# Performance work log

Measured on AMD Instinct MI355X. Metric: run time of the kernel, lower is better.

The kernel has to match this reference:

```python
import jax, jax.numpy as jnp
from jax import lax
import numpy as np

PI = np.float32(np.pi)
DN = ('NCHW', 'OIHW', 'NCHW')
PAD = [(1, 1), (1, 1)]


def setup_inputs() -> dict:
    key = jax.random.key(0)
    k1, k2 = jax.random.split(key, 2)
    B, C, H, W_ = 8, 64, 256, 256
    OUT, K = 64, 8
    x = jax.random.normal(k1, (B, C, H, W_), dtype=jnp.float32)
    # kaiming-normal-like scale for 3x3 conv weights
    W = jax.random.normal(k2, (K, OUT, C, 3, 3), dtype=jnp.float32) * np.float32(np.sqrt(2.0 / (C * 9)))
    b = jnp.zeros((K, OUT), dtype=jnp.float32)  # nn.init.zeros_(conv.bias)
    return {"x": x, "W": W, "b": b}


def reference(x, W, b):
    B, C, H, Wd = x.shape
    K = W.shape[0]
    sx = jnp.array([[1, 0, -1], [2, 0, -2], [1, 0, -1]], dtype=jnp.float32)
    sy = jnp.array([[1, 2, 1], [0, 0, 0], [-1, -2, -1]], dtype=jnp.float32)
    kx = jnp.tile(sx[None, None], (C, 1, 1, 1))  # (C,1,3,3) depthwise
    ky = jnp.tile(sy[None, None], (C, 1, 1, 1))
    grad_x = lax.conv_general_dilated(x, kx, (1, 1), PAD, dimension_numbers=DN, feature_group_count=C)
    grad_y = lax.conv_general_dilated(x, ky, (1, 1), PAD, dimension_numbers=DN, feature_group_count=C)
    theta = jnp.arctan2(grad_y, grad_x)
    # ((theta+pi)/(2pi)*K).long() % K ; values >= 0 so trunc == floor
    q = ((theta + PI) / (2 * PI) * K).astype(jnp.int32) % K  # (B,C,H,W)
    out = jnp.zeros((B, W.shape[1], H, Wd), dtype=x.dtype)
    for k in range(K):
        mask = (q == k).astype(x.dtype)
        fk = lax.conv_general_dilated(x * mask, W[k], (1, 1), PAD, dimension_numbers=DN)
        out = out + fk + b[k][None, :, None, None]
    return out / K
```

## Files before the change

### kernel.cpp

```cpp
#include <hip/hip_runtime.h>
#include <math.h>


#define TH 16
#define TW 32

typedef __attribute__((ext_vector_type(8)))  short    short8;
typedef __attribute__((ext_vector_type(16))) float    f32x16;
typedef __attribute__((ext_vector_type(4)))  unsigned u32x4;

__device__ __forceinline__ float atanf_fdlibm(float x) {
#pragma clang fp contract(off)
    const float atanhi0 = 4.6364760399e-01f, atanhi1 = 7.8539812565e-01f,
                atanhi2 = 9.8279368877e-01f, atanhi3 = 1.5707962513e+00f;
    const float atanlo0 = 5.0121582440e-09f, atanlo1 = 3.7748947079e-08f,
                atanlo2 = 3.4473217170e-08f, atanlo3 = 7.5497894159e-08f;
    const float aT0 = 3.3333334327e-01f, aT1 = -2.0000000298e-01f, aT2 = 1.4285714924e-01f,
                aT3 = -1.1111110449e-01f, aT4 = 9.0908870101e-02f, aT5 = -7.6918758452e-02f,
                aT6 = 6.6610731184e-02f, aT7 = -5.8335702866e-02f, aT8 = 4.9768779427e-02f,
                aT9 = -3.6531571299e-02f, aT10 = 1.6285819933e-02f;

    int hx = __float_as_int(x);
    int ix = hx & 0x7fffffff;
    int id;
    if (ix >= 0x4c800000) {
        if (ix > 0x7f800000) return x + x;
        return (hx > 0) ? (atanhi3 + atanlo3) : (-atanhi3 - atanlo3);
    }
    if (ix < 0x3ee00000) {
        if (ix < 0x31000000) return x;
        id = -1;
    } else {
        x = fabsf(x);
        if (ix < 0x3f980000) {
            if (ix < 0x3f300000) { id = 0; x = (2.0f * x - 1.0f) / (2.0f + x); }
            else                 { id = 1; x = (x - 1.0f) / (x + 1.0f); }
        } else {
            if (ix < 0x401c0000) { id = 2; x = (x - 1.5f) / (1.0f + 1.5f * x); }
            else                 { id = 3; x = -1.0f / x; }
        }
    }
    float z = x * x;
    float w = z * z;
    float s1 = z * (aT0 + w * (aT2 + w * (aT4 + w * (aT6 + w * (aT8 + w * aT10)))));
    float s2 = w * (aT1 + w * (aT3 + w * (aT5 + w * (aT7 + w * aT9))));
    if (id < 0) return x - x * (s1 + s2);
    float r;
    if      (id == 0) r = atanhi0 - ((x * (s1 + s2) - atanlo0) - x);
    else if (id == 1) r = atanhi1 - ((x * (s1 + s2) - atanlo1) - x);
    else if (id == 2) r = atanhi2 - ((x * (s1 + s2) - atanlo2) - x);
    else              r = atanhi3 - ((x * (s1 + s2) - atanlo3) - x);
    return (hx < 0) ? -r : r;
}

__device__ __forceinline__ float atan2f_fdlibm(float y, float x) {
#pragma clang fp contract(off)
    const float tiny = 1.0e-30f;
    const float pi_o_4 = 7.8539818525e-01f;
    const float pi_o_2 = 1.5707963705e+00f;
    const float pi     = 3.1415927410e+00f;
    const float pi_lo  = -8.7422776573e-08f;

    int hx = __float_as_int(x), hy = __float_as_int(y);
    int ix = hx & 0x7fffffff, iy = hy & 0x7fffffff;
    if (ix > 0x7f800000 || iy > 0x7f800000) return x + y;
    if (hx == 0x3f800000) return atanf_fdlibm(y);
    int m = ((hy >> 31) & 1) | ((hx >> 30) & 2);

    if (iy == 0) {
        switch (m) {
            case 0:
            case 1:  return y;
            case 2:  return  pi + tiny;
            default: return -pi - tiny;
        }
    }
    if (ix == 0) return (hy < 0) ? (-pi_o_2 - tiny) : (pi_o_2 + tiny);
    if (ix == 0x7f800000) {
        if (iy == 0x7f800000) {
            switch (m) {
                case 0:  return  pi_o_4 + tiny;
                case 1:  return -pi_o_4 - tiny;
                case 2:  return  3.0f * pi_o_4 + tiny;
                default: return -3.0f * pi_o_4 - tiny;
            }
        } else {
            switch (m) {
                case 0:  return  0.0f;
                case 1:  return -0.0f;
                case 2:  return  pi + tiny;
                default: return -pi - tiny;
            }
        }
    }
    if (iy == 0x7f800000) return (hy < 0) ? (-pi_o_2 - tiny) : (pi_o_2 + tiny);

    int k = (iy - ix) >> 23;
    float z;
    int mm = m;
    if (k > 26)                    { z = pi_o_2 + 0.5f * pi_lo; mm &= 1; }
    else if (hx < 0 && k < -26)    { z = 0.0f; }
    else                           { z = atanf_fdlibm(fabsf(y / x)); }

    switch (mm) {
        case 0:  return z;
        case 1:  return -z;
        case 2:  return pi - (z - pi_lo);
        default: return (z - pi_lo) - pi;
    }
}

__device__ __forceinline__ int bin8(float gy, float gx) {
#pragma clang fp contract(off)
    float th = atan2f_fdlibm(gy, gx);
    float t  = th + 3.14159274101257324f;
    float u  = t / 6.28318548202514648f;
    u = u * 8.0f;
    return ((int)u) & 7;
}

__device__ __forceinline__ int bin8_bf(float gy, float gx) {
#pragma clang fp contract(off)
    const float aT0 = 3.3333334327e-01f, aT1 = -2.0000000298e-01f, aT2 = 1.4285714924e-01f,
                aT3 = -1.1111110449e-01f, aT4 = 9.0908870101e-02f, aT5 = -7.6918758452e-02f,
                aT6 = 6.6610731184e-02f, aT7 = -5.8335702866e-02f, aT8 = 4.9768779427e-02f,
                aT9 = -3.6531571299e-02f, aT10 = 1.6285819933e-02f;
    const float pi    = 3.1415927410e+00f;
    const float pi_lo = -8.7422776573e-08f;
    const float pio2  = 1.5707963705e+00f;

    int hx = __float_as_int(gx), hy = __float_as_int(gy);
    int ix = hx & 0x7fffffff,   iy = hy & 0x7fffffff;
    int m  = ((hy >> 31) & 1) | ((hx >> 30) & 2);

    float q  = fabsf(gy / gx);
    int   iq = __float_as_int(q);

    bool lt04375 = iq < 0x3ee00000;
    bool lt06875 = iq < 0x3f300000;
    bool lt11875 = iq < 0x3f980000;
    bool lt24375 = iq < 0x401c0000;

    float n0 = 2.0f * q - 1.0f, d0 = 2.0f + q;
    float n1 = q - 1.0f,        d1 = q + 1.0f;
    float n2 = q - 1.5f,        d2 = 1.0f + 1.5f * q;
    float num = lt04375 ? q    : lt06875 ? n0 : lt11875 ? n1 : lt24375 ? n2 : -1.0f;
    float den = lt04375 ? 1.0f : lt06875 ? d0 : lt11875 ? d1 : lt24375 ? d2 : q;
    float hi  = lt06875 ? 4.6364760399e-01f : lt11875 ? 7.8539812565e-01f
              : lt24375 ? 9.8279368877e-01f : 1.5707962513e+00f;
    float lo  = lt06875 ? 5.0121582440e-09f : lt11875 ? 3.7748947079e-08f
              : lt24375 ? 3.4473217170e-08f : 7.5497894159e-08f;

    float a  = num / den;
    float z2 = a * a;
    float w2 = z2 * z2;
    float s1 = z2 * (aT0 + w2 * (aT2 + w2 * (aT4 + w2 * (aT6 + w2 * (aT8 + w2 * aT10)))));
    float s2 = w2 * (aT1 + w2 * (aT3 + w2 * (aT5 + w2 * (aT7 + w2 * aT9))));
    float S  = s1 + s2;
    float resm1 = a - a * S;
    float resid = hi - ((a * S - lo) - a);
    float zr = lt04375 ? resm1 : resid;
    zr = (iq >= 0x4c800000) ? (1.5707962513e+00f + 7.5497894159e-08f) : zr;

    int  k    = (iy - ix) >> 23;
    bool kbig = k > 26;
    float z   = kbig ? (pio2 + 0.5f * pi_lo) : zr;
    z = (hx < 0 && k < -26) ? 0.0f : z;
    int mm = kbig ? (m & 1) : m;

    float w  = z - pi_lo;
    float r2 = pi - w;
    float r3 = w - pi;
    float res = (mm == 0) ? z : (mm == 1) ? -z : (mm == 2) ? r2 : r3;
    res = (ix == 0) ? ((hy < 0) ? -pio2 : pio2) : res;
    float piy = (m == 2) ? pi : (m == 3) ? -pi : gy;
    res = (iy == 0) ? piy : res;

    float t = res + 3.14159274101257324f;
    float u = t / 6.28318548202514648f;
    u = u * 8.0f;
    return ((int)u) & 7;
}

__device__ __forceinline__ unsigned rne_bf16_bits(float f) {
    unsigned u = __float_as_uint(f);
    return (u + 0x7fffu + ((u >> 16) & 1u)) >> 16;
}

__global__ __launch_bounds__(256)
void bin_kernel(const float* __restrict__ x, unsigned* __restrict__ pwg) {
    __shared__ float rs[3][260];
    const int w    = threadIdx.x;
    const int hrow = blockIdx.x;
    const int img  = blockIdx.y;
    const float* xim = x + ((size_t)img << 16);
    #pragma unroll
    for (int r = 0; r < 3; ++r) {
        int gh = hrow - 1 + r;
        float v = 0.f;
        if ((unsigned)gh < 256u) v = xim[(gh << 8) + w];
        rs[r][w + 1] = v;
        if (w == 0) { rs[r][0] = 0.f; rs[r][257] = 0.f; }
    }
    __syncthreads();
    int q; unsigned hv;
    {
#pragma clang fp contract(off)
        float a0 = rs[0][w], a1 = rs[0][w + 1], a2 = rs[0][w + 2];
        float m0 = rs[1][w],                    m2 = rs[1][w + 2];
        float z0 = rs[2][w], z1 = rs[2][w + 1], z2 = rs[2][w + 2];
        float gx = ((((a0 - a2) + 2.0f * m0) - 2.0f * m2) + z0) - z2;
        float gy = ((((a0 + 2.0f * a1) + a2) - z0) - 2.0f * z1) - z2;
        q  = bin8_bf(gy, gx);
        hv = rne_bf16_bits(rs[1][w + 1]);
    }
    pwg[((size_t)img << 16) + (hrow << 8) + w] = (hv << 16) | (unsigned)q;
}

__global__ void prep_w2(const float* __restrict__ Wg, short* __restrict__ wsw) {
    int tid = blockIdx.x * 256 + threadIdx.x;
    if (tid >= 4096) return;
    int c = tid >> 6, o = tid & 63;
    for (int t = 0; t < 9; ++t)
        #pragma unroll
        for (int k = 0; k < 8; ++k)
            wsw[((((c * 10 + t) << 6) + o) << 3) + k] =
                (short)rne_bf16_bits(Wg[(((k << 6) + o) * 64 + c) * 9 + t]);
    #pragma unroll
    for (int k = 0; k < 8; ++k)
        wsw[((((c * 10 + 9) << 6) + o) << 3) + k] = 0;
}

__device__ __forceinline__ void build_oh(unsigned pv, u32x4* dst) {
    unsigned q  = pv & 7u;
    unsigned hv = (q & 1u) ? (pv & 0xffff0000u) : (pv >> 16);
    unsigned s2 = q >> 1;
    u32x4 oh;
    oh.x = (s2 == 0u) ? hv : 0u;
    oh.y = (s2 == 1u) ? hv : 0u;
    oh.z = (s2 == 2u) ? hv : 0u;
    oh.w = (s2 == 3u) ? hv : 0u;
    *dst = oh;
}

__global__ __launch_bounds__(256, 2)
void dirconv_mfma2(const unsigned* __restrict__ pwg,
                   const short*    __restrict__ wsw,
                   const float*    __restrict__ bg,
                   float*          __restrict__ out) {
    __shared__ u32x4 pwx[2][648];
    __shared__ u32x4 wl2[2][640];
    __shared__ float bsum[64];

    const int tid  = threadIdx.x;
    const int wave = tid >> 6;
    const int lane = tid & 63;
    const int h    = lane >> 5;
    const int l31  = lane & 31;
    const int bb   = blockIdx.z;
    const int h0   = blockIdx.y * TH;
    const int w0c  = blockIdx.x * TW;

    if (tid < 64) {
        float s = 0.f;
        #pragma unroll
        for (int k = 0; k < 8; ++k) s += bg[k * 64 + tid];
        bsum[tid] = s;
    }

    f32x16 acc[2][4];
    #pragma unroll
    for (int i = 0; i < 2; ++i)
        #pragma unroll
        for (int j = 0; j < 4; ++j)
            acc[i][j] = (f32x16)0.f;

    int rro[5], c2o[5];
    #pragma unroll
    for (int s = 0; s < 5; ++s) {
        int t = 2 * s + h;
        int t3 = t / 3;
        rro[s] = (t <= 8) ? t3 : 0;
        c2o[s] = (t <= 8) ? (t - t3 * 3) : 0;
    }

    {
        const u32x4* wsrc = (const u32x4*)wsw;
        wl2[0][tid]       = wsrc[tid];
        wl2[0][tid + 256] = wsrc[tid + 256];
        if (tid < 128) wl2[0][tid + 512] = wsrc[tid + 512];
        const unsigned* pimg = pwg + ((size_t)(bb * 64) << 16);
        #pragma unroll
        for (int rd = 0; rd < 3; ++rd) {
            int idx = tid + rd * 256;
            if (idx < 612) {
                int r = idx / 34, cc2 = idx - r * 34;
                int gh = h0 + r - 1, gw = w0c + cc2 - 1;
                unsigned pv = 0;
                if ((unsigned)gh < 256u && (unsigned)gw < 256u)
                    pv = pimg[(gh << 8) + gw];
                build_oh(pv, &pwx[0][r * 36 + cc2]);
            }
        }
    }
    __syncthreads();

    for (int c = 0; c < 64; ++c) {
        const int cb = c & 1, nb = cb ^ 1;
        u32x4 wv0 = (u32x4)0u, wv1 = (u32x4)0u, wv2 = (u32x4)0u;
        unsigned pv0 = 0, pv1 = 0, pv2 = 0;
        const bool more = (c < 63);

        if (more) {
            const u32x4* wsrc = (const u32x4*)(wsw + (size_t)(c + 1) * 5120);
            wv0 = wsrc[tid];
            wv1 = wsrc[tid + 256];
            if (tid < 128) wv2 = wsrc[tid + 512];
            const unsigned* pimg = pwg + ((size_t)(bb * 64 + c + 1) << 16);
            {   int idx = tid;       int r = idx / 34, cc2 = idx - r * 34;
                int gh = h0 + r - 1, gw = w0c + cc2 - 1;
                if ((unsigned)gh < 256u && (unsigned)gw < 256u) pv0 = pimg[(gh << 8) + gw]; }
            {   int idx = tid + 256; int r = idx / 34, cc2 = idx - r * 34;
                int gh = h0 + r - 1, gw = w0c + cc2 - 1;
                if ((unsigned)gh < 256u && (unsigned)gw < 256u) pv1 = pimg[(gh << 8) + gw]; }
            if (tid < 100) {
                int idx = tid + 512; int r = idx / 34, cc2 = idx - r * 34;
                int gh = h0 + r - 1, gw = w0c + cc2 - 1;
                if ((unsigned)gh < 256u && (unsigned)gw < 256u) pv2 = pimg[(gh << 8) + gw]; }
        }

        const u32x4* pb = &pwx[cb][0];
        const u32x4* wb = &wl2[cb][0];
        auto mfma_step = [&](int s) {
            const int t = 2 * s + h;
            short8 a0 = __builtin_bit_cast(short8, wb[t * 64 + l31]);
            short8 a1 = __builtin_bit_cast(short8, wb[t * 64 + 32 + l31]);
            #pragma unroll
            for (int nf = 0; nf < 4; ++nf) {
                int py = wave * 4 + nf;
                short8 bf = __builtin_bit_cast(short8,
                                pb[(py + rro[s]) * 36 + l31 + c2o[s]]);
                acc[0][nf] = __builtin_amdgcn_mfma_f32_32x32x16_bf16(a0, bf, acc[0][nf], 0, 0, 0);
                acc[1][nf] = __builtin_amdgcn_mfma_f32_32x32x16_bf16(a1, bf, acc[1][nf], 0, 0, 0);
            }
        };

        __builtin_amdgcn_s_setprio(1);
        mfma_step(0);
        mfma_step(1);
        __builtin_amdgcn_s_setprio(0);
        if (more) {
            wl2[nb][tid]       = wv0;
            wl2[nb][tid + 256] = wv1;
            if (tid < 128) wl2[nb][tid + 512] = wv2;
        }
        __builtin_amdgcn_s_setprio(1);
        mfma_step(2);
        __builtin_amdgcn_s_setprio(0);
        if (more) {
            {   int idx = tid;       int r = idx / 34, cc2 = idx - r * 34;
                build_oh(pv0, &pwx[nb][r * 36 + cc2]); }
            {   int idx = tid + 256; int r = idx / 34, cc2 = idx - r * 34;
                build_oh(pv1, &pwx[nb][r * 36 + cc2]); }
        }
        __builtin_amdgcn_s_setprio(1);
        mfma_step(3);
        __builtin_amdgcn_s_setprio(0);
        if (more && tid < 100) {
            int idx = tid + 512; int r = idx / 34, cc2 = idx - r * 34;
            build_oh(pv2, &pwx[nb][r * 36 + cc2]);
        }
        __builtin_amdgcn_s_setprio(1);
        mfma_step(4);
        __builtin_amdgcn_s_setprio(0);
        __syncthreads();
    }

    float* ob = out + ((size_t)bb << 22);
    #pragma unroll
    for (int mf = 0; mf < 2; ++mf)
        #pragma unroll
        for (int nf = 0; nf < 4; ++nf) {
            int py = wave * 4 + nf;
            #pragma unroll
            for (int reg = 0; reg < 16; ++reg) {
                int o = mf * 32 + (reg & 3) + 8 * (reg >> 2) + 4 * h;
                ob[((size_t)o << 16) + ((h0 + py) << 8) + (w0c + l31)] =
                    (acc[mf][nf][reg] + bsum[o]) * 0.125f;
            }
        }
}

__global__ __launch_bounds__(256, 2)
void dirconv_fb(const float* __restrict__ x,
                const float* __restrict__ Wg,
                const float* __restrict__ bg,
                float* __restrict__ out) {
    __shared__ float    xs[20 * 37];
    __shared__ unsigned pw[18 * 36];
    __shared__ short    wl[64][128];
    __shared__ float    bsum[64];

    const int tid  = threadIdx.x;
    const int wave = tid >> 6;
    const int lane = tid & 63;
    const int h    = lane >> 5;
    const int l31  = lane & 31;
    const int bb   = blockIdx.z;
    const int h0   = blockIdx.y * TH;
    const int w0   = blockIdx.x * TW;

    if (tid < 64) {
        float s = 0.f;
        #pragma unroll
        for (int k = 0; k < 8; ++k) s += bg[k * 64 + tid];
        bsum[tid] = s;
    }

    f32x16 acc[2][4];
    #pragma unroll
    for (int i = 0; i < 2; ++i)
        #pragma unroll
        for (int j = 0; j < 4; ++j)
            acc[i][j] = (f32x16)0.f;

    const int swz0 = l31 & 7;

    for (int c = 0; c < 64; ++c) {
        __syncthreads();
        const float* xc = x + ((size_t)(bb * 64 + c) << 16);
        for (int idx = tid; idx < 720; idx += 256) {
            int r = idx / 36, cc = idx - r * 36;
            int gh = h0 + r - 2, gw = w0 + cc - 2;
            float v = 0.f;
            if ((unsigned)gh < 256u && (unsigned)gw < 256u)
                v = xc[(gh << 8) + gw];
            xs[r * 37 + cc] = v;
        }
        for (int pair = tid; pair < 512; pair += 256) {
            int k = pair >> 6, o = pair & 63;
            const float* g = Wg + ((size_t)((k << 6) + o) * 64 + c) * 9;
            #pragma unroll
            for (int t = 0; t < 9; ++t)
                wl[o][((t ^ (o & 7)) << 3) + k] = (short)rne_bf16_bits(g[t]);
        }
        if (tid < 64) {
            int o = tid;
            #pragma unroll
            for (int e = 0; e < 8; ++e) wl[o][((9 ^ (o & 7)) << 3) + e] = 0;
        }
        __syncthreads();

        for (int idx = tid; idx < 612; idx += 256) {
            int r = idx / 34, cc = idx - r * 34;
            const float* p0 = &xs[r * 37 + cc];
            int q; unsigned hv;
            {
#pragma clang fp contract(off)
                float a0 = p0[0],  a1 = p0[1],  a2 = p0[2];
                float m0 = p0[37],              m2 = p0[39];
                float z0 = p0[74], z1 = p0[75], z2 = p0[76];
                float gx = ((((a0 - a2) + 2.0f * m0) - 2.0f * m2) + z0) - z2;
                float gy = ((((a0 + 2.0f * a1) + a2) - z0) - 2.0f * z1) - z2;
                q  = bin8(gy, gx);
                hv = rne_bf16_bits(p0[38]);
            }
            pw[r * 36 + cc] = (hv << 16) | (unsigned)q;
        }
        __syncthreads();

        #pragma unroll
        for (int s = 0; s < 5; ++s) {
            const int t = 2 * s + h;
            short8 a0 = *(const short8*)&wl[l31     ][(t ^ swz0) << 3];
            short8 a1 = *(const short8*)&wl[32 + l31][(t ^ swz0) << 3];
            const int t3 = t / 3;
            const int dy = t3 - 1, dx = t - t3 * 3 - 1;
            const bool val = (t <= 8);
            #pragma unroll
            for (int nf = 0; nf < 4; ++nf) {
                int py = wave * 4 + nf;
                int rr = val ? (py + 1 + dy) : 0;
                int c2 = val ? (l31 + 1 + dx) : 0;
                unsigned pv = pw[rr * 36 + c2];
                pv = val ? pv : 0u;
                unsigned q   = pv & 7u;
                unsigned hhi = pv & 0xffff0000u;
                unsigned hlo = pv >> 16;
                u32x4 bw;
                bw.x = (q == 0u ? hlo : 0u) | (q == 1u ? hhi : 0u);
                bw.y = (q == 2u ? hlo : 0u) | (q == 3u ? hhi : 0u);
                bw.z = (q == 4u ? hlo : 0u) | (q == 5u ? hhi : 0u);
                bw.w = (q == 6u ? hlo : 0u) | (q == 7u ? hhi : 0u);
                short8 bf = __builtin_bit_cast(short8, bw);
                acc[0][nf] = __builtin_amdgcn_mfma_f32_32x32x16_bf16(a0, bf, acc[0][nf], 0, 0, 0);
                acc[1][nf] = __builtin_amdgcn_mfma_f32_32x32x16_bf16(a1, bf, acc[1][nf], 0, 0, 0);
            }
        }
    }

    float* ob = out + ((size_t)bb << 22);
    #pragma unroll
    for (int mf = 0; mf < 2; ++mf)
        #pragma unroll
        for (int nf = 0; nf < 4; ++nf) {
            int py = wave * 4 + nf;
            #pragma unroll
            for (int reg = 0; reg < 16; ++reg) {
                int o = mf * 32 + (reg & 3) + 8 * (reg >> 2) + 4 * h;
                ob[((size_t)o << 16) + ((h0 + py) << 8) + (w0 + l31)] =
                    (acc[mf][nf][reg] + bsum[o]) * 0.125f;
            }
        }
}

extern "C" void kernel_launch(void* const* d_in, const int* in_sizes, int n_in,
                              void* d_out, int out_size, void* d_ws, size_t ws_size,
                              hipStream_t stream) {
    const float* x  = (const float*)d_in[0];
    const float* Wg = (const float*)d_in[1];
    const float* bg = (const float*)d_in[2];
    float* out = (float*)d_out;

    dim3 grid(256 / TW, 256 / TH, 8);
    dim3 block(256);

    const size_t pw_bytes   = (size_t)8 * 64 * 256 * 256 * 4;
    const size_t wsw2_bytes = (size_t)64 * 10 * 64 * 8 * 2;

    if (ws_size >= pw_bytes + wsw2_bytes) {
        unsigned* pwg = (unsigned*)d_ws;
        short*    wsw = (short*)((char*)d_ws + pw_bytes);
        bin_kernel<<<dim3(256, 512, 1), 256, 0, stream>>>(x, pwg);
        prep_w2<<<16, 256, 0, stream>>>(Wg, wsw);
        dirconv_mfma2<<<grid, block, 0, stream>>>(pwg, wsw, bg, out);
    } else {
        dirconv_fb<<<grid, block, 0, stream>>>(x, Wg, bg, out);
    }
}
```

Before: 416.0 us.

## Halve conv tile height, load weights directly into registers, batch bin kernel rows

The main conv kernel now works on 8-row tiles with half the accumulators per wave, targeting 3 blocks per CU. It drops the LDS weight double-buffer and instead loads each MFMA step's A fragments straight from global memory into ping-pong registers, one step ahead. The bin kernel now processes 16 rows per block from an 18-row LDS tile, which cuts redundant halo loads. In exchange, each tile reloads a larger share of halo rows and every step depends on global weight-load latency being hidden behind the MFMAs.

```diff
diff --git a/kernel.cpp b/kernel.cpp
--- a/kernel.cpp
+++ b/kernel.cpp
@@ -2,7 +2,7 @@
 #include <math.h>
 
 
-#define TH 16
+#define TH 8
 #define TW 32
 
 typedef __attribute__((ext_vector_type(8)))  short    short8;
@@ -188,33 +188,34 @@
 }
 
 __global__ __launch_bounds__(256)
-void bin_kernel(const float* __restrict__ x, unsigned* __restrict__ pwg) {
-    __shared__ float rs[3][260];
-    const int w    = threadIdx.x;
-    const int hrow = blockIdx.x;
-    const int img  = blockIdx.y;
+void bin_kernel2(const float* __restrict__ x, unsigned* __restrict__ pwg) {
+    __shared__ float rs[18][260];
+    const int w   = threadIdx.x;
+    const int r0  = blockIdx.x << 4;
+    const int img = blockIdx.y;
     const float* xim = x + ((size_t)img << 16);
     #pragma unroll
-    for (int r = 0; r < 3; ++r) {
-        int gh = hrow - 1 + r;
-        float v = 0.f;
-        if ((unsigned)gh < 256u) v = xim[(gh << 8) + w];
-        rs[r][w + 1] = v;
-        if (w == 0) { rs[r][0] = 0.f; rs[r][257] = 0.f; }
-    }
+    for (int r = 0; r < 18; ++r) {
+        int gh = r0 + r - 1;
+        rs[r][w + 1] = ((unsigned)gh < 256u) ? xim[(gh << 8) + w] : 0.f;
+    }
+    if (w < 18) { rs[w][0] = 0.f; rs[w][257] = 0.f; }
     __syncthreads();
-    int q; unsigned hv;
-    {
+    unsigned* orow = pwg + ((size_t)img << 16) + (r0 << 8) + w;
+    for (int rr = 0; rr < 16; ++rr) {
+        int q; unsigned hv;
+        {
 #pragma clang fp contract(off)
-        float a0 = rs[0][w], a1 = rs[0][w + 1], a2 = rs[0][w + 2];
-        float m0 = rs[1][w],                    m2 = rs[1][w + 2];
-        float z0 = rs[2][w], z1 = rs[2][w + 1], z2 = rs[2][w + 2];
-        float gx = ((((a0 - a2) + 2.0f * m0) - 2.0f * m2) + z0) - z2;
-        float gy = ((((a0 + 2.0f * a1) + a2) - z0) - 2.0f * z1) - z2;
-        q  = bin8_bf(gy, gx);
-        hv = rne_bf16_bits(rs[1][w + 1]);
-    }
-    pwg[((size_t)img << 16) + (hrow << 8) + w] = (hv << 16) | (unsigned)q;
+            float a0 = rs[rr][w],     a1 = rs[rr][w + 1],     a2 = rs[rr][w + 2];
+            float m0 = rs[rr + 1][w],                         m2 = rs[rr + 1][w + 2];
+            float z0 = rs[rr + 2][w], z1 = rs[rr + 2][w + 1], z2 = rs[rr + 2][w + 2];
+            float gx = ((((a0 - a2) + 2.0f * m0) - 2.0f * m2) + z0) - z2;
+            float gy = ((((a0 + 2.0f * a1) + a2) - z0) - 2.0f * z1) - z2;
+            q  = bin8_bf(gy, gx);
+            hv = rne_bf16_bits(rs[rr + 1][w + 1]);
+        }
+        orow[rr << 8] = (hv << 16) | (unsigned)q;
+    }
 }
 
 __global__ void prep_w2(const float* __restrict__ Wg, short* __restrict__ wsw) {
@@ -243,13 +244,65 @@
     *dst = oh;
 }
 
-__global__ __launch_bounds__(256, 2)
-void dirconv_mfma2(const unsigned* __restrict__ pwg,
+#define WLOAD(DST, CC, SS) do {                                                      \
+    int t_ = 2 * (SS) + h;                                                           \
+    const u32x4* wp_ = (const u32x4*)(wsw + (size_t)((((CC) * 10 + t_) << 6)) * 8);  \
+    DST[0] = wp_[l31];                                                               \
+    DST[1] = wp_[32 + l31];                                                          \
+} while (0)
+
+#define MSTEP(P, SS) do {                                                            \
+    __builtin_amdgcn_s_setprio(1);                                                   \
+    short8 a0_ = __builtin_bit_cast(short8, P[0]);                                   \
+    short8 a1_ = __builtin_bit_cast(short8, P[1]);                                   \
+    _Pragma("unroll")                                                                \
+    for (int nf = 0; nf < 2; ++nf) {                                                 \
+        int py_ = (wave << 1) + nf;                                                  \
+        short8 bf_ = __builtin_bit_cast(short8,                                      \
+                         pb[(py_ + rro[SS]) * 36 + l31 + c2o[SS]]);                  \
+        acc[0][nf] = __builtin_amdgcn_mfma_f32_32x32x16_bf16(a0_, bf_, acc[0][nf], 0, 0, 0); \
+        acc[1][nf] = __builtin_amdgcn_mfma_f32_32x32x16_bf16(a1_, bf_, acc[1][nf], 0, 0, 0); \
+    }                                                                                \
+    __builtin_amdgcn_s_setprio(0);                                                   \
+} while (0)
+
+#define CBODY(C, P, Q) do {                                                          \
+    const int  cb_ = (C) & 1, nb_ = cb_ ^ 1;                                         \
+    const int  cn_ = ((C) < 63) ? (C) + 1 : 63;                                      \
+    const bool more_ = (C) < 63;                                                     \
+    unsigned pv0_ = 0, pv1_ = 0;                                                     \
+    if (more_) {                                                                     \
+        const unsigned* pimg_ = pwg + ((size_t)(bb * 64 + (C) + 1) << 16);           \
+        { int r_ = tid / 34, cc_ = tid - r_ * 34;                                    \
+          int gh_ = h0 + r_ - 1, gw_ = w0c + cc_ - 1;                                \
+          if ((unsigned)gh_ < 256u && (unsigned)gw_ < 256u)                          \
+              pv0_ = pimg_[(gh_ << 8) + gw_]; }                                      \
+        if (tid < 84) { int i_ = tid + 256; int r_ = i_ / 34, cc_ = i_ - r_ * 34;    \
+          int gh_ = h0 + r_ - 1, gw_ = w0c + cc_ - 1;                                \
+          if ((unsigned)gh_ < 256u && (unsigned)gw_ < 256u)                          \
+              pv1_ = pimg_[(gh_ << 8) + gw_]; }                                      \
+    }                                                                                \
+    const u32x4* pb = &pwx[cb_][0];                                                  \
+    MSTEP(P, 0);  WLOAD(P, (C), 2);                                                  \
+    MSTEP(Q, 1);  WLOAD(Q, (C), 3);                                                  \
+    MSTEP(P, 2);  WLOAD(P, (C), 4);                                                  \
+    if (more_) {                                                                     \
+        { int r_ = tid / 34, cc_ = tid - r_ * 34;                                    \
+          build_oh(pv0_, &pwx[nb_][r_ * 36 + cc_]); }                                \
+        if (tid < 84) { int i_ = tid + 256; int r_ = i_ / 34, cc_ = i_ - r_ * 34;    \
+          build_oh(pv1_, &pwx[nb_][r_ * 36 + cc_]); }                                \
+    }                                                                                \
+    MSTEP(Q, 3);  WLOAD(Q, cn_, 0);                                                  \
+    MSTEP(P, 4);  WLOAD(P, cn_, 1);                                                  \
+    __syncthreads();                                                                 \
+} while (0)
+
+__global__ __launch_bounds__(256, 3)
+void dirconv_mfma3(const unsigned* __restrict__ pwg,
                    const short*    __restrict__ wsw,
                    const float*    __restrict__ bg,
                    float*          __restrict__ out) {
-    __shared__ u32x4 pwx[2][648];
-    __shared__ u32x4 wl2[2][640];
+    __shared__ u32x4 pwx[2][360];
     __shared__ float bsum[64];
 
     const int tid  = threadIdx.x;
@@ -268,11 +321,11 @@
         bsum[tid] = s;
     }
 
-    f32x16 acc[2][4];
+    f32x16 acc[2][2];
     #pragma unroll
     for (int i = 0; i < 2; ++i)
         #pragma unroll
-        for (int j = 0; j < 4; ++j)
+        for (int j = 0; j < 2; ++j)
             acc[i][j] = (f32x16)0.f;
 
     int rro[5], c2o[5];
@@ -284,104 +337,36 @@
         c2o[s] = (t <= 8) ? (t - t3 * 3) : 0;
     }
 
+    u32x4 A0[2], A1[2];
+
     {
-        const u32x4* wsrc = (const u32x4*)wsw;
-        wl2[0][tid]       = wsrc[tid];
-        wl2[0][tid + 256] = wsrc[tid + 256];
-        if (tid < 128) wl2[0][tid + 512] = wsrc[tid + 512];
         const unsigned* pimg = pwg + ((size_t)(bb * 64) << 16);
-        #pragma unroll
-        for (int rd = 0; rd < 3; ++rd) {
-            int idx = tid + rd * 256;
-            if (idx < 612) {
-                int r = idx / 34, cc2 = idx - r * 34;
-                int gh = h0 + r - 1, gw = w0c + cc2 - 1;
-                unsigned pv = 0;
-                if ((unsigned)gh < 256u && (unsigned)gw < 256u)
-                    pv = pimg[(gh << 8) + gw];
-                build_oh(pv, &pwx[0][r * 36 + cc2]);
-            }
-        }
+        { int r = tid / 34, cc2 = tid - r * 34;
+          int gh = h0 + r - 1, gw = w0c + cc2 - 1;
+          unsigned pv = 0;
+          if ((unsigned)gh < 256u && (unsigned)gw < 256u) pv = pimg[(gh << 8) + gw];
+          build_oh(pv, &pwx[0][r * 36 + cc2]); }
+        if (tid < 84) { int i = tid + 256; int r = i / 34, cc2 = i - r * 34;
+          int gh = h0 + r - 1, gw = w0c + cc2 - 1;
+          unsigned pv = 0;
+          if ((unsigned)gh < 256u && (unsigned)gw < 256u) pv = pimg[(gh << 8) + gw];
+          build_oh(pv, &pwx[0][r * 36 + cc2]); }
+        WLOAD(A0, 0, 0);
+        WLOAD(A1, 0, 1);
     }
     __syncthreads();
 
-    for (int c = 0; c < 64; ++c) {
-        const int cb = c & 1, nb = cb ^ 1;
-        u32x4 wv0 = (u32x4)0u, wv1 = (u32x4)0u, wv2 = (u32x4)0u;
-        unsigned pv0 = 0, pv1 = 0, pv2 = 0;
-        const bool more = (c < 63);
-
-        if (more) {
-            const u32x4* wsrc = (const u32x4*)(wsw + (size_t)(c + 1) * 5120);
-            wv0 = wsrc[tid];
-            wv1 = wsrc[tid + 256];
-            if (tid < 128) wv2 = wsrc[tid + 512];
-            const unsigned* pimg = pwg + ((size_t)(bb * 64 + c + 1) << 16);
-            {   int idx = tid;       int r = idx / 34, cc2 = idx - r * 34;
-                int gh = h0 + r - 1, gw = w0c + cc2 - 1;
-                if ((unsigned)gh < 256u && (unsigned)gw < 256u) pv0 = pimg[(gh << 8) + gw]; }
-            {   int idx = tid + 256; int r = idx / 34, cc2 = idx - r * 34;
-                int gh = h0 + r - 1, gw = w0c + cc2 - 1;
-                if ((unsigned)gh < 256u && (unsigned)gw < 256u) pv1 = pimg[(gh << 8) + gw]; }
-            if (tid < 100) {
-                int idx = tid + 512; int r = idx / 34, cc2 = idx - r * 34;
-                int gh = h0 + r - 1, gw = w0c + cc2 - 1;
-                if ((unsigned)gh < 256u && (unsigned)gw < 256u) pv2 = pimg[(gh << 8) + gw]; }
-        }
-
-        const u32x4* pb = &pwx[cb][0];
-        const u32x4* wb = &wl2[cb][0];
-        auto mfma_step = [&](int s) {
-            const int t = 2 * s + h;
-            short8 a0 = __builtin_bit_cast(short8, wb[t * 64 + l31]);
-            short8 a1 = __builtin_bit_cast(short8, wb[t * 64 + 32 + l31]);
-            #pragma unroll
-            for (int nf = 0; nf < 4; ++nf) {
-                int py = wave * 4 + nf;
-                short8 bf = __builtin_bit_cast(short8,
-                                pb[(py + rro[s]) * 36 + l31 + c2o[s]]);
-                acc[0][nf] = __builtin_amdgcn_mfma_f32_32x32x16_bf16(a0, bf, acc[0][nf], 0, 0, 0);
-                acc[1][nf] = __builtin_amdgcn_mfma_f32_32x32x16_bf16(a1, bf, acc[1][nf], 0, 0, 0);
-            }
-        };
-
-        __builtin_amdgcn_s_setprio(1);
-        mfma_step(0);
-        mfma_step(1);
-        __builtin_amdgcn_s_setprio(0);
-        if (more) {
-            wl2[nb][tid]       = wv0;
-            wl2[nb][tid + 256] = wv1;
-            if (tid < 128) wl2[nb][tid + 512] = wv2;
-        }
-        __builtin_amdgcn_s_setprio(1);
-        mfma_step(2);
-        __builtin_amdgcn_s_setprio(0);
-        if (more) {
-            {   int idx = tid;       int r = idx / 34, cc2 = idx - r * 34;
-                build_oh(pv0, &pwx[nb][r * 36 + cc2]); }
-            {   int idx = tid + 256; int r = idx / 34, cc2 = idx - r * 34;
-                build_oh(pv1, &pwx[nb][r * 36 + cc2]); }
-        }
-        __builtin_amdgcn_s_setprio(1);
-        mfma_step(3);
-        __builtin_amdgcn_s_setprio(0);
-        if (more && tid < 100) {
-            int idx = tid + 512; int r = idx / 34, cc2 = idx - r * 34;
-            build_oh(pv2, &pwx[nb][r * 36 + cc2]);
-        }
-        __builtin_amdgcn_s_setprio(1);
-        mfma_step(4);
-        __builtin_amdgcn_s_setprio(0);
-        __syncthreads();
+    for (int c2 = 0; c2 < 64; c2 += 2) {
+        CBODY(c2,     A0, A1);
+        CBODY(c2 + 1, A1, A0);
     }
 
     float* ob = out + ((size_t)bb << 22);
     #pragma unroll
     for (int mf = 0; mf < 2; ++mf)
         #pragma unroll
-        for (int nf = 0; nf < 4; ++nf) {
-            int py = wave * 4 + nf;
+        for (int nf = 0; nf < 2; ++nf) {
+            int py = (wave << 1) + nf;
             #pragma unroll
             for (int reg = 0; reg < 16; ++reg) {
                 int o = mf * 32 + (reg & 3) + 8 * (reg >> 2) + 4 * h;
@@ -407,8 +392,8 @@
     const int h    = lane >> 5;
     const int l31  = lane & 31;
     const int bb   = blockIdx.z;
-    const int h0   = blockIdx.y * TH;
-    const int w0   = blockIdx.x * TW;
+    const int h0   = blockIdx.y * 16;
+    const int w0   = blockIdx.x * 32;
 
     if (tid < 64) {
         float s = 0.f;
@@ -522,19 +507,16 @@
     const float* bg = (const float*)d_in[2];
     float* out = (float*)d_out;
 
-    dim3 grid(256 / TW, 256 / TH, 8);
-    dim3 block(256);
-
     const size_t pw_bytes   = (size_t)8 * 64 * 256 * 256 * 4;
     const size_t wsw2_bytes = (size_t)64 * 10 * 64 * 8 * 2;
 
     if (ws_size >= pw_bytes + wsw2_bytes) {
         unsigned* pwg = (unsigned*)d_ws;
         short*    wsw = (short*)((char*)d_ws + pw_bytes);
-        bin_kernel<<<dim3(256, 512, 1), 256, 0, stream>>>(x, pwg);
+        bin_kernel2<<<dim3(16, 512, 1), 256, 0, stream>>>(x, pwg);
         prep_w2<<<16, 256, 0, stream>>>(Wg, wsw);
-        dirconv_mfma2<<<grid, block, 0, stream>>>(pwg, wsw, bg, out);
+        dirconv_mfma3<<<dim3(256 / TW, 256 / TH, 8), 256, 0, stream>>>(pwg, wsw, bg, out);
     } else {
-        dirconv_fb<<<grid, block, 0, stream>>>(x, Wg, bg, out);
-    }
-}
+        dirconv_fb<<<dim3(8, 16, 8), 256, 0, stream>>>(x, Wg, bg, out);
+    }
+}
```

After: 417.7 us. About the same (+0.4%).

## Halve conv tile height for four blocks per CU and batch bin rows

Applied to the files above, without the earlier changes.

The MFMA conv kernel now uses 8-row tiles with half the accumulators per wave and launch bounds of 4 blocks per CU, so more blocks fit per CU and latency hiding improves. The interleaved staging of next-channel data between MFMA steps is replaced by a plain loop followed by a single LDS store phase. The bin kernel now processes 16 rows per block from a shared 18-row strip, cutting redundant halo loads and block count. The trade-off is more halo overhead per output in the conv tiles and less overlap of LDS writes with MFMA work.

```diff
diff --git a/kernel.cpp b/kernel.cpp
--- a/kernel.cpp
+++ b/kernel.cpp
@@ -2,7 +2,7 @@
 #include <math.h>
 
 
-#define TH 16
+#define TH 8
 #define TW 32
 
 typedef __attribute__((ext_vector_type(8)))  short    short8;
@@ -188,33 +188,34 @@
 }
 
 __global__ __launch_bounds__(256)
-void bin_kernel(const float* __restrict__ x, unsigned* __restrict__ pwg) {
-    __shared__ float rs[3][260];
-    const int w    = threadIdx.x;
-    const int hrow = blockIdx.x;
-    const int img  = blockIdx.y;
+void bin_kernel2(const float* __restrict__ x, unsigned* __restrict__ pwg) {
+    __shared__ float rs[18][260];
+    const int w   = threadIdx.x;
+    const int r0  = blockIdx.x << 4;
+    const int img = blockIdx.y;
     const float* xim = x + ((size_t)img << 16);
     #pragma unroll
-    for (int r = 0; r < 3; ++r) {
-        int gh = hrow - 1 + r;
-        float v = 0.f;
-        if ((unsigned)gh < 256u) v = xim[(gh << 8) + w];
-        rs[r][w + 1] = v;
-        if (w == 0) { rs[r][0] = 0.f; rs[r][257] = 0.f; }
-    }
+    for (int r = 0; r < 18; ++r) {
+        int gh = r0 + r - 1;
+        rs[r][w + 1] = ((unsigned)gh < 256u) ? xim[(gh << 8) + w] : 0.f;
+    }
+    if (w < 18) { rs[w][0] = 0.f; rs[w][257] = 0.f; }
     __syncthreads();
-    int q; unsigned hv;
-    {
+    unsigned* orow = pwg + ((size_t)img << 16) + (r0 << 8) + w;
+    for (int rr = 0; rr < 16; ++rr) {
+        int q; unsigned hv;
+        {
 #pragma clang fp contract(off)
-        float a0 = rs[0][w], a1 = rs[0][w + 1], a2 = rs[0][w + 2];
-        float m0 = rs[1][w],                    m2 = rs[1][w + 2];
-        float z0 = rs[2][w], z1 = rs[2][w + 1], z2 = rs[2][w + 2];
-        float gx = ((((a0 - a2) + 2.0f * m0) - 2.0f * m2) + z0) - z2;
-        float gy = ((((a0 + 2.0f * a1) + a2) - z0) - 2.0f * z1) - z2;
-        q  = bin8_bf(gy, gx);
-        hv = rne_bf16_bits(rs[1][w + 1]);
-    }
-    pwg[((size_t)img << 16) + (hrow << 8) + w] = (hv << 16) | (unsigned)q;
+            float a0 = rs[rr][w],     a1 = rs[rr][w + 1],     a2 = rs[rr][w + 2];
+            float m0 = rs[rr + 1][w],                         m2 = rs[rr + 1][w + 2];
+            float z0 = rs[rr + 2][w], z1 = rs[rr + 2][w + 1], z2 = rs[rr + 2][w + 2];
+            float gx = ((((a0 - a2) + 2.0f * m0) - 2.0f * m2) + z0) - z2;
+            float gy = ((((a0 + 2.0f * a1) + a2) - z0) - 2.0f * z1) - z2;
+            q  = bin8_bf(gy, gx);
+            hv = rne_bf16_bits(rs[rr + 1][w + 1]);
+        }
+        orow[rr << 8] = (hv << 16) | (unsigned)q;
+    }
 }
 
 __global__ void prep_w2(const float* __restrict__ Wg, short* __restrict__ wsw) {
@@ -243,12 +244,12 @@
     *dst = oh;
 }
 
-__global__ __launch_bounds__(256, 2)
-void dirconv_mfma2(const unsigned* __restrict__ pwg,
+__global__ __launch_bounds__(256, 4)
+void dirconv_mfma4(const unsigned* __restrict__ pwg,
                    const short*    __restrict__ wsw,
                    const float*    __restrict__ bg,
                    float*          __restrict__ out) {
-    __shared__ u32x4 pwx[2][648];
+    __shared__ u32x4 pwx[2][360];
     __shared__ u32x4 wl2[2][640];
     __shared__ float bsum[64];
 
@@ -268,11 +269,11 @@
         bsum[tid] = s;
     }
 
-    f32x16 acc[2][4];
+    f32x16 acc[2][2];
     #pragma unroll
     for (int i = 0; i < 2; ++i)
         #pragma unroll
-        for (int j = 0; j < 4; ++j)
+        for (int j = 0; j < 2; ++j)
             acc[i][j] = (f32x16)0.f;
 
     int rro[5], c2o[5];
@@ -283,6 +284,10 @@
         rro[s] = (t <= 8) ? t3 : 0;
         c2o[s] = (t <= 8) ? (t - t3 * 3) : 0;
     }
+
+    const int r0_ = tid / 34, c0_ = tid - r0_ * 34;
+    const int i1_ = tid + 256;
+    const int r1_ = i1_ / 34, c1_ = i1_ - r1_ * 34;
 
     {
         const u32x4* wsrc = (const u32x4*)wsw;
@@ -290,26 +295,26 @@
         wl2[0][tid + 256] = wsrc[tid + 256];
         if (tid < 128) wl2[0][tid + 512] = wsrc[tid + 512];
         const unsigned* pimg = pwg + ((size_t)(bb * 64) << 16);
-        #pragma unroll
-        for (int rd = 0; rd < 3; ++rd) {
-            int idx = tid + rd * 256;
-            if (idx < 612) {
-                int r = idx / 34, cc2 = idx - r * 34;
-                int gh = h0 + r - 1, gw = w0c + cc2 - 1;
-                unsigned pv = 0;
-                if ((unsigned)gh < 256u && (unsigned)gw < 256u)
-                    pv = pimg[(gh << 8) + gw];
-                build_oh(pv, &pwx[0][r * 36 + cc2]);
-            }
+        {
+            int gh = h0 + r0_ - 1, gw = w0c + c0_ - 1;
+            unsigned pv = 0;
+            if ((unsigned)gh < 256u && (unsigned)gw < 256u) pv = pimg[(gh << 8) + gw];
+            build_oh(pv, &pwx[0][r0_ * 36 + c0_]);
+        }
+        if (tid < 84) {
+            int gh = h0 + r1_ - 1, gw = w0c + c1_ - 1;
+            unsigned pv = 0;
+            if ((unsigned)gh < 256u && (unsigned)gw < 256u) pv = pimg[(gh << 8) + gw];
+            build_oh(pv, &pwx[0][r1_ * 36 + c1_]);
         }
     }
     __syncthreads();
 
     for (int c = 0; c < 64; ++c) {
         const int cb = c & 1, nb = cb ^ 1;
+        const bool more = (c < 63);
         u32x4 wv0 = (u32x4)0u, wv1 = (u32x4)0u, wv2 = (u32x4)0u;
-        unsigned pv0 = 0, pv1 = 0, pv2 = 0;
-        const bool more = (c < 63);
+        unsigned pv0 = 0, pv1 = 0;
 
         if (more) {
             const u32x4* wsrc = (const u32x4*)(wsw + (size_t)(c + 1) * 5120);
@@ -317,62 +322,42 @@
             wv1 = wsrc[tid + 256];
             if (tid < 128) wv2 = wsrc[tid + 512];
             const unsigned* pimg = pwg + ((size_t)(bb * 64 + c + 1) << 16);
-            {   int idx = tid;       int r = idx / 34, cc2 = idx - r * 34;
-                int gh = h0 + r - 1, gw = w0c + cc2 - 1;
-                if ((unsigned)gh < 256u && (unsigned)gw < 256u) pv0 = pimg[(gh << 8) + gw]; }
-            {   int idx = tid + 256; int r = idx / 34, cc2 = idx - r * 34;
-                int gh = h0 + r - 1, gw = w0c + cc2 - 1;
-                if ((unsigned)gh < 256u && (unsigned)gw < 256u) pv1 = pimg[(gh << 8) + gw]; }
-            if (tid < 100) {
-                int idx = tid + 512; int r = idx / 34, cc2 = idx - r * 34;
-                int gh = h0 + r - 1, gw = w0c + cc2 - 1;
-                if ((unsigned)gh < 256u && (unsigned)gw < 256u) pv2 = pimg[(gh << 8) + gw]; }
+            {
+                int gh = h0 + r0_ - 1, gw = w0c + c0_ - 1;
+                if ((unsigned)gh < 256u && (unsigned)gw < 256u) pv0 = pimg[(gh << 8) + gw];
+            }
+            if (tid < 84) {
+                int gh = h0 + r1_ - 1, gw = w0c + c1_ - 1;
+                if ((unsigned)gh < 256u && (unsigned)gw < 256u) pv1 = pimg[(gh << 8) + gw];
+            }
         }
 
         const u32x4* pb = &pwx[cb][0];
         const u32x4* wb = &wl2[cb][0];
-        auto mfma_step = [&](int s) {
+        #pragma unroll
+        for (int s = 0; s < 5; ++s) {
             const int t = 2 * s + h;
             short8 a0 = __builtin_bit_cast(short8, wb[t * 64 + l31]);
             short8 a1 = __builtin_bit_cast(short8, wb[t * 64 + 32 + l31]);
+            __builtin_amdgcn_s_setprio(1);
             #pragma unroll
-            for (int nf = 0; nf < 4; ++nf) {
-                int py = wave * 4 + nf;
+            for (int nf = 0; nf < 2; ++nf) {
+                int py = (wave << 1) + nf;
                 short8 bf = __builtin_bit_cast(short8,
                                 pb[(py + rro[s]) * 36 + l31 + c2o[s]]);
                 acc[0][nf] = __builtin_amdgcn_mfma_f32_32x32x16_bf16(a0, bf, acc[0][nf], 0, 0, 0);
                 acc[1][nf] = __builtin_amdgcn_mfma_f32_32x32x16_bf16(a1, bf, acc[1][nf], 0, 0, 0);
             }
-        };
-
-        __builtin_amdgcn_s_setprio(1);
-        mfma_step(0);
-        mfma_step(1);
-        __builtin_amdgcn_s_setprio(0);
+            __builtin_amdgcn_s_setprio(0);
+        }
+
         if (more) {
             wl2[nb][tid]       = wv0;
             wl2[nb][tid + 256] = wv1;
             if (tid < 128) wl2[nb][tid + 512] = wv2;
-        }
-        __builtin_amdgcn_s_setprio(1);
-        mfma_step(2);
-        __builtin_amdgcn_s_setprio(0);
-        if (more) {
-            {   int idx = tid;       int r = idx / 34, cc2 = idx - r * 34;
-                build_oh(pv0, &pwx[nb][r * 36 + cc2]); }
-            {   int idx = tid + 256; int r = idx / 34, cc2 = idx - r * 34;
-                build_oh(pv1, &pwx[nb][r * 36 + cc2]); }
-        }
-        __builtin_amdgcn_s_setprio(1);
-        mfma_step(3);
-        __builtin_amdgcn_s_setprio(0);
-        if (more && tid < 100) {
-            int idx = tid + 512; int r = idx / 34, cc2 = idx - r * 34;
-            build_oh(pv2, &pwx[nb][r * 36 + cc2]);
-        }
-        __builtin_amdgcn_s_setprio(1);
-        mfma_step(4);
-        __builtin_amdgcn_s_setprio(0);
+            build_oh(pv0, &pwx[nb][r0_ * 36 + c0_]);
+            if (tid < 84) build_oh(pv1, &pwx[nb][r1_ * 36 + c1_]);
+        }
         __syncthreads();
     }
 
@@ -380,8 +365,8 @@
     #pragma unroll
     for (int mf = 0; mf < 2; ++mf)
         #pragma unroll
-        for (int nf = 0; nf < 4; ++nf) {
-            int py = wave * 4 + nf;
+        for (int nf = 0; nf < 2; ++nf) {
+            int py = (wave << 1) + nf;
             #pragma unroll
             for (int reg = 0; reg < 16; ++reg) {
                 int o = mf * 32 + (reg & 3) + 8 * (reg >> 2) + 4 * h;
@@ -407,8 +392,8 @@
     const int h    = lane >> 5;
     const int l31  = lane & 31;
     const int bb   = blockIdx.z;
-    const int h0   = blockIdx.y * TH;
-    const int w0   = blockIdx.x * TW;
+    const int h0   = blockIdx.y * 16;
+    const int w0   = blockIdx.x * 32;
 
     if (tid < 64) {
         float s = 0.f;
@@ -522,19 +507,16 @@
     const float* bg = (const float*)d_in[2];
     float* out = (float*)d_out;
 
-    dim3 grid(256 / TW, 256 / TH, 8);
-    dim3 block(256);
-
     const size_t pw_bytes   = (size_t)8 * 64 * 256 * 256 * 4;
     const size_t wsw2_bytes = (size_t)64 * 10 * 64 * 8 * 2;
 
     if (ws_size >= pw_bytes + wsw2_bytes) {
         unsigned* pwg = (unsigned*)d_ws;
         short*    wsw = (short*)((char*)d_ws + pw_bytes);
-        bin_kernel<<<dim3(256, 512, 1), 256, 0, stream>>>(x, pwg);
+        bin_kernel2<<<dim3(16, 512, 1), 256, 0, stream>>>(x, pwg);
         prep_w2<<<16, 256, 0, stream>>>(Wg, wsw);
-        dirconv_mfma2<<<grid, block, 0, stream>>>(pwg, wsw, bg, out);
+        dirconv_mfma4<<<dim3(256 / TW, 256 / TH, 8), 256, 0, stream>>>(pwg, wsw, bg, out);
     } else {
-        dirconv_fb<<<grid, block, 0, stream>>>(x, Wg, bg, out);
-    }
-}
+        dirconv_fb<<<dim3(8, 16, 8), 256, 0, stream>>>(x, Wg, bg, out);
+    }
+}
```

Measured after the change: 398.6 us. 4.2% less time.
